# Kernel optimization log

Measured on AMD Instinct MI355X. Metric: run time of the kernel, lower is better.

## Reference

```python
import jax, jax.numpy as jnp
import numpy as np

N_NODES = 50000


def _gcn_norm(edge_index, num_nodes):
    # PyG gcn_norm with add_self_loops=True, edge_weight=1
    loops = jnp.arange(num_nodes, dtype=edge_index.dtype)
    src = jnp.concatenate([edge_index[0], loops])
    dst = jnp.concatenate([edge_index[1], loops])
    deg = jax.ops.segment_sum(jnp.ones_like(dst, dtype=jnp.float32), dst,
                              num_segments=num_nodes)
    deg_inv_sqrt = jnp.where(deg > 0, jax.lax.rsqrt(jnp.maximum(deg, 1.0)), 0.0)
    norm = deg_inv_sqrt[src] * deg_inv_sqrt[dst]  # [E + N]
    return src, dst, norm


def _gcn_conv(x, src, dst, norm, W, b, num_nodes):
    h = x @ W                                 # [N, out] dense transform first
    msg = h[src] * norm[:, None]              # gather + scale, [E+N, out]
    out = jax.ops.segment_sum(msg, dst, num_segments=num_nodes)  # scatter-add
    return out + b


def setup_inputs() -> dict:
    key = jax.random.key(0)
    k1, k2, k3, k4, k5 = jax.random.split(key, 5)
    in_ch, out_ch = 128, 64
    hid = 2 * out_ch
    x = jax.random.normal(k1, (N_NODES, in_ch), dtype=jnp.float32)
    edge_index = jax.random.randint(k2, (2, 800000), 0, N_NODES, dtype=jnp.int64)
    # Glorot init like PyG GCNConv
    W1 = jax.random.normal(k3, (in_ch, hid), dtype=jnp.float32) * (1.0 / np.sqrt(in_ch))
    b1 = jnp.zeros((hid,), dtype=jnp.float32)
    W2 = jax.random.normal(k4, (hid, out_ch), dtype=jnp.float32) * (1.0 / np.sqrt(hid))
    b2 = jnp.zeros((out_ch,), dtype=jnp.float32)
    return {"x": x, "edge_index": edge_index, "W1": W1, "b1": b1,
            "W2": W2, "b2": b2}


def reference(x, edge_index, W1, b1, W2, b2):
    num_nodes = x.shape[0]
    src, dst, norm = _gcn_norm(edge_index, num_nodes)
    h = _gcn_conv(x, src, dst, norm, W1, b1, num_nodes)
    h = jax.nn.relu(h)
    return _gcn_conv(h, src, dst, norm, W2, b2, num_nodes)
```

## Files before the change

### kernel.cpp

```cpp
#include <hip/hip_runtime.h>

#define N_NODES 50000
#define N_EDGES 800000
#define IN_CH   128
#define HID     128
#define OUT_CH  64

#define NBUCK 196
#define BCAP  5120
#define XPAD  136

#define G1_BLOCKS ((N_NODES + 63) / 64)
#define GSPLIT 391

typedef __attribute__((ext_vector_type(8))) short bf16x8;
typedef __attribute__((ext_vector_type(4))) float f32x4;
typedef unsigned short ushort_t;

__device__ __forceinline__ unsigned short f2bf(float f) {
    unsigned u = __float_as_uint(f);
    u += 0x7fffu + ((u >> 16) & 1u);
    return (unsigned short)(u >> 16);
}
__device__ __forceinline__ unsigned pack2(float a, float b) {
    return (unsigned)f2bf(a) | ((unsigned)f2bf(b) << 16);
}
__device__ __forceinline__ float bf_lo(unsigned u) { return __uint_as_float(u << 16); }
__device__ __forceinline__ float bf_hi(unsigned u) { return __uint_as_float(u & 0xffff0000u); }


__global__ __launch_bounds__(256) void k_prep(const float* __restrict__ W1,
                                              const float* __restrict__ W2,
                                              ushort_t* __restrict__ W1t,
                                              ushort_t* __restrict__ W2t,
                                              int* __restrict__ bcur) {
    if (blockIdx.x == 0 && threadIdx.x < NBUCK) bcur[threadIdx.x] = 0;
    int i = blockIdx.x * 256 + threadIdx.x;
    if (i < 128 * 128) {
        int k = i >> 7, c = i & 127;
        W1t[c * 128 + k] = f2bf(W1[k * 128 + c]);
    } else {
        int j = i - 128 * 128;
        if (j < 128 * 64) {
            int k = j >> 6, c = j & 63;
            W2t[c * 128 + k] = f2bf(W2[k * 64 + c]);
        }
    }
}


__global__ __launch_bounds__(256) void k_stage(const int phase, const int tile0,
                                               const int* __restrict__ src,
                                               const int* __restrict__ dst,
                                               int* __restrict__ bcur,
                                               unsigned* __restrict__ rec,
                                               const float* __restrict__ x,
                                               const ushort_t* __restrict__ W1t,
                                               ushort_t* __restrict__ g,
                                               int* __restrict__ row_beg,
                                               int* __restrict__ row_end,
                                               float* __restrict__ dis,
                                               int* __restrict__ col) {
    __shared__ char smem[52224];
    const int tid = threadIdx.x;

    if (blockIdx.x < NBUCK) {
        if (phase == 0) {
            int* lh    = (int*)smem;
            int* gbase = (int*)(smem + 1024);
            for (int i = tid; i < NBUCK; i += 256) lh[i] = 0;
            __syncthreads();
            int base = blockIdx.x * 4096;
#pragma unroll 4
            for (int k = 0; k < 16; ++k) {
                int e = base + k * 256 + tid;
                if (e < N_EDGES) atomicAdd(&lh[dst[e] >> 8], 1);
            }
            __syncthreads();
            for (int i = tid; i < NBUCK; i += 256) {
                int c = lh[i];
                gbase[i] = c ? (i * BCAP + atomicAdd(&bcur[i], c)) : 0;
            }
            __syncthreads();
            for (int i = tid; i < NBUCK; i += 256) lh[i] = 0;
            __syncthreads();
#pragma unroll 4
            for (int k = 0; k < 16; ++k) {
                int e = base + k * 256 + tid;
                if (e < N_EDGES) {
                    int d = dst[e], b = d >> 8;
                    int rk = atomicAdd(&lh[b], 1);
                    int pos = gbase[b] + rk;
                    if (pos < (b + 1) * BCAP)
                        rec[pos] = (unsigned)src[e] | ((unsigned)(d & 255) << 16);
                }
            }
        } else {
            int* lh  = (int*)smem;
            int* cur = lh + 256;
            int* s   = cur + 256;
            const int b = blockIdx.x, t = tid;
            const int lo = b * BCAP;
            const int cnt = min(bcur[b], BCAP);
            const int hi = lo + cnt;

            lh[t] = 0;
            __syncthreads();
            for (int j = lo + t; j < hi; j += 256)
                atomicAdd(&lh[rec[j] >> 16], 1);
            __syncthreads();
            int deg = lh[t];
            s[t] = deg;
            __syncthreads();
            for (int off = 1; off < 256; off <<= 1) {
                int u = (t >= off) ? s[t - off] : 0;
                __syncthreads();
                s[t] += u;
                __syncthreads();
            }
            int gp = lo + s[t] - deg;
            int node = (b << 8) + t;
            if (node < N_NODES) {
                row_beg[node] = gp;
                row_end[node] = gp + deg;
                dis[node] = rsqrtf((float)deg + 1.0f);
            }
            cur[t] = gp;
            __syncthreads();
            for (int j = lo + t; j < hi; j += 256) {
                unsigned r = rec[j];
                int pos = atomicAdd(&cur[r >> 16], 1);
                col[pos] = (int)(r & 0xffffu);
            }
        }
    } else {
        ushort_t* xs = (ushort_t*)smem;
        ushort_t* ws = (ushort_t*)(smem + 17408);
        const int bid = tile0 + (blockIdx.x - NBUCK);
        const int row0 = bid * 64;

        for (int i = tid; i < 64 * 32; i += 256) {
            int r = i >> 5, k4 = (i & 31) << 2;
            int gr = row0 + r;
            float4 v = make_float4(0.f, 0.f, 0.f, 0.f);
            if (gr < N_NODES) v = *(const float4*)&x[(long)gr * IN_CH + k4];
            ushort4 u;
            u.x = f2bf(v.x); u.y = f2bf(v.y); u.z = f2bf(v.z); u.w = f2bf(v.w);
            *(ushort4*)&xs[r * XPAD + k4] = u;
        }
        for (int i = tid; i < 128 * 16; i += 256) {
            int c = i >> 4, seg = i & 15;
            *(uint4*)&ws[c * XPAD + seg * 8] = *(const uint4*)&W1t[c * 128 + seg * 8];
        }
        __syncthreads();

        const int w = tid >> 6, lane = tid & 63;
        const int m = lane & 15, q = lane >> 4;
        const ushort_t* arow = &xs[(w * 16 + m) * XPAD + q * 8];
        const ushort_t* brow = &ws[m * XPAD + q * 8];

        f32x4 acc[8] = {};
#pragma unroll
        for (int k0 = 0; k0 < 128; k0 += 32) {
            bf16x8 a = *(const bf16x8*)(arow + k0);
#pragma unroll
            for (int nt = 0; nt < 8; ++nt) {
                bf16x8 b = *(const bf16x8*)(brow + nt * 16 * XPAD + k0);
                acc[nt] = __builtin_amdgcn_mfma_f32_16x16x32_bf16(a, b, acc[nt], 0, 0, 0);
            }
        }

#pragma unroll
        for (int reg = 0; reg < 4; ++reg) {
            int gr = row0 + w * 16 + q * 4 + reg;
            if (gr < N_NODES) {
#pragma unroll
                for (int nt = 0; nt < 8; ++nt)
                    g[(long)gr * HID + nt * 16 + m] = f2bf(acc[nt][reg]);
            }
        }
    }
}


__global__ __launch_bounds__(256) void k_agg1(const int* __restrict__ row_beg,
                                              const int* __restrict__ row_end,
                                              const int* __restrict__ col,
                                              const float* __restrict__ dis,
                                              const ushort_t* __restrict__ g1,
                                              const float* __restrict__ b1,
                                              ushort_t* __restrict__ a1) {
    int r = blockIdx.x * 4 + (threadIdx.x >> 6);
    if (r >= N_NODES) return;
    const int lane = threadIdx.x & 63;
    const int q = lane >> 4;
    const int seg = lane & 15;
    const int cl = seg << 3;
    const uint4* G = (const uint4*)g1;
    const int beg = row_beg[r], end = row_end[r];

    float acc[8] = {};
    int e = beg + q;
    for (; e + 4 < end; e += 8) {
        int s0 = col[e], s1 = col[e + 4];
        float d0 = dis[s0], d1 = dis[s1];
        uint4 u0 = G[(long)s0 * 16 + seg];
        uint4 u1 = G[(long)s1 * 16 + seg];
        acc[0] += bf_lo(u0.x) * d0; acc[1] += bf_hi(u0.x) * d0;
        acc[2] += bf_lo(u0.y) * d0; acc[3] += bf_hi(u0.y) * d0;
        acc[4] += bf_lo(u0.z) * d0; acc[5] += bf_hi(u0.z) * d0;
        acc[6] += bf_lo(u0.w) * d0; acc[7] += bf_hi(u0.w) * d0;
        acc[0] += bf_lo(u1.x) * d1; acc[1] += bf_hi(u1.x) * d1;
        acc[2] += bf_lo(u1.y) * d1; acc[3] += bf_hi(u1.y) * d1;
        acc[4] += bf_lo(u1.z) * d1; acc[5] += bf_hi(u1.z) * d1;
        acc[6] += bf_lo(u1.w) * d1; acc[7] += bf_hi(u1.w) * d1;
    }
    if (e < end) {
        int s0 = col[e];
        float d0 = dis[s0];
        uint4 u = G[(long)s0 * 16 + seg];
        acc[0] += bf_lo(u.x) * d0; acc[1] += bf_hi(u.x) * d0;
        acc[2] += bf_lo(u.y) * d0; acc[3] += bf_hi(u.y) * d0;
        acc[4] += bf_lo(u.z) * d0; acc[5] += bf_hi(u.z) * d0;
        acc[6] += bf_lo(u.w) * d0; acc[7] += bf_hi(u.w) * d0;
    }
#pragma unroll
    for (int off = 16; off < 64; off <<= 1)
#pragma unroll
        for (int j = 0; j < 8; ++j) acc[j] += __shfl_xor(acc[j], off);

    if (q == 0) {
        const float d = dis[r];
        uint4 u = G[(long)r * 16 + seg];
        acc[0] += bf_lo(u.x) * d; acc[1] += bf_hi(u.x) * d;
        acc[2] += bf_lo(u.y) * d; acc[3] += bf_hi(u.y) * d;
        acc[4] += bf_lo(u.z) * d; acc[5] += bf_hi(u.z) * d;
        acc[6] += bf_lo(u.w) * d; acc[7] += bf_hi(u.w) * d;
        float o[8];
#pragma unroll
        for (int j = 0; j < 8; ++j) o[j] = fmaxf(acc[j] * d + b1[cl + j], 0.f);
        uint4 pw;
        pw.x = pack2(o[0], o[1]); pw.y = pack2(o[2], o[3]);
        pw.z = pack2(o[4], o[5]); pw.w = pack2(o[6], o[7]);
        *(uint4*)&a1[(long)r * HID + cl] = pw;
    }
}


__global__ __launch_bounds__(256) void k_gemm2(const ushort_t* __restrict__ a1,
                                               const ushort_t* __restrict__ W2t,
                                               const float* __restrict__ dis,
                                               ushort_t* __restrict__ g) {
    __shared__ ushort_t xs[64 * XPAD];
    __shared__ ushort_t ws[64 * XPAD];
    const int tid = threadIdx.x;
    const int row0 = blockIdx.x * 64;

    for (int i = tid; i < 64 * 16; i += 256) {
        int r = i >> 4, seg = i & 15;
        int gr = row0 + r;
        uint4 v = make_uint4(0u, 0u, 0u, 0u);
        if (gr < N_NODES) v = *(const uint4*)&a1[(long)gr * HID + seg * 8];
        *(uint4*)&xs[r * XPAD + seg * 8] = v;
    }
    for (int i = tid; i < 64 * 16; i += 256) {
        int c = i >> 4, seg = i & 15;
        *(uint4*)&ws[c * XPAD + seg * 8] = *(const uint4*)&W2t[c * 128 + seg * 8];
    }
    __syncthreads();

    const int w = tid >> 6, lane = tid & 63;
    const int m = lane & 15, q = lane >> 4;
    const ushort_t* arow = &xs[(w * 16 + m) * XPAD + q * 8];
    const ushort_t* brow = &ws[m * XPAD + q * 8];

    f32x4 acc[4] = {};
#pragma unroll
    for (int k0 = 0; k0 < 128; k0 += 32) {
        bf16x8 a = *(const bf16x8*)(arow + k0);
#pragma unroll
        for (int nt = 0; nt < 4; ++nt) {
            bf16x8 b = *(const bf16x8*)(brow + nt * 16 * XPAD + k0);
            acc[nt] = __builtin_amdgcn_mfma_f32_16x16x32_bf16(a, b, acc[nt], 0, 0, 0);
        }
    }

#pragma unroll
    for (int reg = 0; reg < 4; ++reg) {
        int gr = row0 + w * 16 + q * 4 + reg;
        if (gr < N_NODES) {
            float d = dis[gr];
#pragma unroll
            for (int nt = 0; nt < 4; ++nt)
                g[(long)gr * OUT_CH + nt * 16 + m] = f2bf(acc[nt][reg] * d);
        }
    }
}


__global__ __launch_bounds__(256) void k_agg2(const int* __restrict__ row_beg,
                                              const int* __restrict__ row_end,
                                              const int* __restrict__ col,
                                              const float* __restrict__ dis,
                                              const ushort_t* __restrict__ g3,
                                              const float* __restrict__ b2,
                                              float* __restrict__ out) {
    int r = blockIdx.x * 4 + (threadIdx.x >> 6);
    if (r >= N_NODES) return;
    const int lane = threadIdx.x & 63;
    const int q = lane >> 3;
    const int seg = lane & 7;
    const int cl = seg << 3;
    const uint4* G = (const uint4*)g3;
    const int beg = row_beg[r], end = row_end[r];

    float acc[8] = {};
    int e = beg + q;
    for (; e + 8 < end; e += 16) {
        int s0 = col[e], s1 = col[e + 8];
        uint4 u0 = G[(long)s0 * 8 + seg];
        uint4 u1 = G[(long)s1 * 8 + seg];
        acc[0] += bf_lo(u0.x); acc[1] += bf_hi(u0.x);
        acc[2] += bf_lo(u0.y); acc[3] += bf_hi(u0.y);
        acc[4] += bf_lo(u0.z); acc[5] += bf_hi(u0.z);
        acc[6] += bf_lo(u0.w); acc[7] += bf_hi(u0.w);
        acc[0] += bf_lo(u1.x); acc[1] += bf_hi(u1.x);
        acc[2] += bf_lo(u1.y); acc[3] += bf_hi(u1.y);
        acc[4] += bf_lo(u1.z); acc[5] += bf_hi(u1.z);
        acc[6] += bf_lo(u1.w); acc[7] += bf_hi(u1.w);
    }
    if (e < end) {
        int s = col[e];
        uint4 u = G[(long)s * 8 + seg];
        acc[0] += bf_lo(u.x); acc[1] += bf_hi(u.x);
        acc[2] += bf_lo(u.y); acc[3] += bf_hi(u.y);
        acc[4] += bf_lo(u.z); acc[5] += bf_hi(u.z);
        acc[6] += bf_lo(u.w); acc[7] += bf_hi(u.w);
    }
#pragma unroll
    for (int off = 8; off < 64; off <<= 1)
#pragma unroll
        for (int j = 0; j < 8; ++j) acc[j] += __shfl_xor(acc[j], off);

    if (q == 0) {
        uint4 u = G[(long)r * 8 + seg];
        acc[0] += bf_lo(u.x); acc[1] += bf_hi(u.x);
        acc[2] += bf_lo(u.y); acc[3] += bf_hi(u.y);
        acc[4] += bf_lo(u.z); acc[5] += bf_hi(u.z);
        acc[6] += bf_lo(u.w); acc[7] += bf_hi(u.w);
        const float d = dis[r];
        float4 o0, o1;
        o0.x = acc[0] * d + b2[cl + 0];
        o0.y = acc[1] * d + b2[cl + 1];
        o0.z = acc[2] * d + b2[cl + 2];
        o0.w = acc[3] * d + b2[cl + 3];
        o1.x = acc[4] * d + b2[cl + 4];
        o1.y = acc[5] * d + b2[cl + 5];
        o1.z = acc[6] * d + b2[cl + 6];
        o1.w = acc[7] * d + b2[cl + 7];
        *(float4*)&out[(long)r * OUT_CH + cl] = o0;
        *(float4*)&out[(long)r * OUT_CH + cl + 4] = o1;
    }
}


extern "C" void kernel_launch(void* const* d_in, const int* in_sizes, int n_in,
                              void* d_out, int out_size, void* d_ws, size_t ws_size,
                              hipStream_t stream) {
    const float* x   = (const float*)d_in[0];
    const int*   ei  = (const int*)d_in[1];
    const float* W1  = (const float*)d_in[2];
    const float* b1  = (const float*)d_in[3];
    const float* W2  = (const float*)d_in[4];
    const float* b2  = (const float*)d_in[5];
    float* out = (float*)d_out;

    const int* src = ei;
    const int* dst = ei + N_EDGES;

    char* p = (char*)d_ws;
    unsigned* rec = (unsigned*)p;         p += (long)NBUCK * BCAP * 4;
    int* col     = (int*)p;               p += (long)NBUCK * BCAP * 4;
    int* row_beg = (int*)p;               p += 50048 * 4;
    int* row_end = (int*)p;               p += 50048 * 4;
    int* bcur    = (int*)p;               p += 256 * 4;
    float* dis   = (float*)p;             p += 50048 * 4;
    ushort_t* W1t = (ushort_t*)p;         p += 128 * 128 * 2;
    ushort_t* W2t = (ushort_t*)p;         p += 128 * 64 * 2;
    ushort_t* g1  = (ushort_t*)p;         p += (long)N_NODES * HID * 2;
    ushort_t* a1  = (ushort_t*)p;         p += (long)N_NODES * HID * 2;
    ushort_t* g3  = (ushort_t*)p;

    const int B = 256;

    k_prep<<<96, B, 0, stream>>>(W1, W2, W1t, W2t, bcur);
    k_stage<<<NBUCK + GSPLIT, B, 0, stream>>>(0, 0, src, dst, bcur, rec,
                                              x, W1t, g1, row_beg, row_end, dis, col);
    k_stage<<<NBUCK + (G1_BLOCKS - GSPLIT), B, 0, stream>>>(1, GSPLIT, src, dst, bcur, rec,
                                              x, W1t, g1, row_beg, row_end, dis, col);
    k_agg1<<<(N_NODES + 3) / 4, B, 0, stream>>>(row_beg, row_end, col, dis, g1, b1, a1);
    k_gemm2<<<(N_NODES + 63) / 64, B, 0, stream>>>(a1, W2t, dis, g3);
    k_agg2<<<(N_NODES + 3) / 4, B, 0, stream>>>(row_beg, row_end, col, dis, g3, b2, out);
}
```

Baseline: 177.3 us.

## Fuse layer-1 aggregation with layer-2 GEMM via shared-memory tile

Merges the first aggregation kernel and the second dense transform into one kernel. Each block aggregates 16 rows (4 per wave), writes the ReLU'd bf16 rows into a shared tile, then runs MFMA against W2 read directly from global memory to produce g3. This removes the a1 round trip through global memory and one kernel launch. In exchange, each wave handles 4 rows serially, which may reduce latency hiding in the gather. W2t is also re-read from global/L2 by every block instead of being staged in LDS.

```diff
diff --git a/kernel.cpp b/kernel.cpp
--- a/kernel.cpp
+++ b/kernel.cpp
@@ -183,117 +183,92 @@
 }
 
 
-__global__ __launch_bounds__(256) void k_agg1(const int* __restrict__ row_beg,
-                                              const int* __restrict__ row_end,
-                                              const int* __restrict__ col,
-                                              const float* __restrict__ dis,
-                                              const ushort_t* __restrict__ g1,
-                                              const float* __restrict__ b1,
-                                              ushort_t* __restrict__ a1) {
-    int r = blockIdx.x * 4 + (threadIdx.x >> 6);
-    if (r >= N_NODES) return;
-    const int lane = threadIdx.x & 63;
+__global__ __launch_bounds__(256) void k_agg1g2(const int* __restrict__ row_beg,
+                                                const int* __restrict__ row_end,
+                                                const int* __restrict__ col,
+                                                const float* __restrict__ dis,
+                                                const ushort_t* __restrict__ g1,
+                                                const float* __restrict__ b1,
+                                                const ushort_t* __restrict__ W2t,
+                                                ushort_t* __restrict__ g3) {
+    __shared__ ushort_t hs[16 * XPAD];
+    const int tid = threadIdx.x;
+    const int w = tid >> 6, lane = tid & 63;
     const int q = lane >> 4;
     const int seg = lane & 15;
     const int cl = seg << 3;
     const uint4* G = (const uint4*)g1;
-    const int beg = row_beg[r], end = row_end[r];
-
-    float acc[8] = {};
-    int e = beg + q;
-    for (; e + 4 < end; e += 8) {
-        int s0 = col[e], s1 = col[e + 4];
-        float d0 = dis[s0], d1 = dis[s1];
-        uint4 u0 = G[(long)s0 * 16 + seg];
-        uint4 u1 = G[(long)s1 * 16 + seg];
-        acc[0] += bf_lo(u0.x) * d0; acc[1] += bf_hi(u0.x) * d0;
-        acc[2] += bf_lo(u0.y) * d0; acc[3] += bf_hi(u0.y) * d0;
-        acc[4] += bf_lo(u0.z) * d0; acc[5] += bf_hi(u0.z) * d0;
-        acc[6] += bf_lo(u0.w) * d0; acc[7] += bf_hi(u0.w) * d0;
-        acc[0] += bf_lo(u1.x) * d1; acc[1] += bf_hi(u1.x) * d1;
-        acc[2] += bf_lo(u1.y) * d1; acc[3] += bf_hi(u1.y) * d1;
-        acc[4] += bf_lo(u1.z) * d1; acc[5] += bf_hi(u1.z) * d1;
-        acc[6] += bf_lo(u1.w) * d1; acc[7] += bf_hi(u1.w) * d1;
-    }
-    if (e < end) {
-        int s0 = col[e];
-        float d0 = dis[s0];
-        uint4 u = G[(long)s0 * 16 + seg];
-        acc[0] += bf_lo(u.x) * d0; acc[1] += bf_hi(u.x) * d0;
-        acc[2] += bf_lo(u.y) * d0; acc[3] += bf_hi(u.y) * d0;
-        acc[4] += bf_lo(u.z) * d0; acc[5] += bf_hi(u.z) * d0;
-        acc[6] += bf_lo(u.w) * d0; acc[7] += bf_hi(u.w) * d0;
-    }
-#pragma unroll
-    for (int off = 16; off < 64; off <<= 1)
-#pragma unroll
-        for (int j = 0; j < 8; ++j) acc[j] += __shfl_xor(acc[j], off);
-
-    if (q == 0) {
-        const float d = dis[r];
-        uint4 u = G[(long)r * 16 + seg];
-        acc[0] += bf_lo(u.x) * d; acc[1] += bf_hi(u.x) * d;
-        acc[2] += bf_lo(u.y) * d; acc[3] += bf_hi(u.y) * d;
-        acc[4] += bf_lo(u.z) * d; acc[5] += bf_hi(u.z) * d;
-        acc[6] += bf_lo(u.w) * d; acc[7] += bf_hi(u.w) * d;
-        float o[8];
-#pragma unroll
-        for (int j = 0; j < 8; ++j) o[j] = fmaxf(acc[j] * d + b1[cl + j], 0.f);
-        uint4 pw;
-        pw.x = pack2(o[0], o[1]); pw.y = pack2(o[2], o[3]);
-        pw.z = pack2(o[4], o[5]); pw.w = pack2(o[6], o[7]);
-        *(uint4*)&a1[(long)r * HID + cl] = pw;
-    }
-}
-
-
-__global__ __launch_bounds__(256) void k_gemm2(const ushort_t* __restrict__ a1,
-                                               const ushort_t* __restrict__ W2t,
-                                               const float* __restrict__ dis,
-                                               ushort_t* __restrict__ g) {
-    __shared__ ushort_t xs[64 * XPAD];
-    __shared__ ushort_t ws[64 * XPAD];
-    const int tid = threadIdx.x;
-    const int row0 = blockIdx.x * 64;
-
-    for (int i = tid; i < 64 * 16; i += 256) {
-        int r = i >> 4, seg = i & 15;
-        int gr = row0 + r;
-        uint4 v = make_uint4(0u, 0u, 0u, 0u);
-        if (gr < N_NODES) v = *(const uint4*)&a1[(long)gr * HID + seg * 8];
-        *(uint4*)&xs[r * XPAD + seg * 8] = v;
-    }
-    for (int i = tid; i < 64 * 16; i += 256) {
-        int c = i >> 4, seg = i & 15;
-        *(uint4*)&ws[c * XPAD + seg * 8] = *(const uint4*)&W2t[c * 128 + seg * 8];
+    const int r0 = blockIdx.x * 16;
+
+    for (int rr = 0; rr < 4; ++rr) {
+        const int r = r0 + w * 4 + rr;
+        const int beg = row_beg[r], end = row_end[r];
+
+        float acc[8] = {};
+        int e = beg + q;
+        for (; e + 4 < end; e += 8) {
+            int s0 = col[e], s1 = col[e + 4];
+            float d0 = dis[s0], d1 = dis[s1];
+            uint4 u0 = G[(long)s0 * 16 + seg];
+            uint4 u1 = G[(long)s1 * 16 + seg];
+            acc[0] += bf_lo(u0.x) * d0; acc[1] += bf_hi(u0.x) * d0;
+            acc[2] += bf_lo(u0.y) * d0; acc[3] += bf_hi(u0.y) * d0;
+            acc[4] += bf_lo(u0.z) * d0; acc[5] += bf_hi(u0.z) * d0;
+            acc[6] += bf_lo(u0.w) * d0; acc[7] += bf_hi(u0.w) * d0;
+            acc[0] += bf_lo(u1.x) * d1; acc[1] += bf_hi(u1.x) * d1;
+            acc[2] += bf_lo(u1.y) * d1; acc[3] += bf_hi(u1.y) * d1;
+            acc[4] += bf_lo(u1.z) * d1; acc[5] += bf_hi(u1.z) * d1;
+            acc[6] += bf_lo(u1.w) * d1; acc[7] += bf_hi(u1.w) * d1;
+        }
+        if (e < end) {
+            int s0 = col[e];
+            float d0 = dis[s0];
+            uint4 u = G[(long)s0 * 16 + seg];
+            acc[0] += bf_lo(u.x) * d0; acc[1] += bf_hi(u.x) * d0;
+            acc[2] += bf_lo(u.y) * d0; acc[3] += bf_hi(u.y) * d0;
+            acc[4] += bf_lo(u.z) * d0; acc[5] += bf_hi(u.z) * d0;
+            acc[6] += bf_lo(u.w) * d0; acc[7] += bf_hi(u.w) * d0;
+        }
+#pragma unroll
+        for (int off = 16; off < 64; off <<= 1)
+#pragma unroll
+            for (int j = 0; j < 8; ++j) acc[j] += __shfl_xor(acc[j], off);
+
+        if (q == 0) {
+            const float d = dis[r];
+            uint4 u = G[(long)r * 16 + seg];
+            acc[0] += bf_lo(u.x) * d; acc[1] += bf_hi(u.x) * d;
+            acc[2] += bf_lo(u.y) * d; acc[3] += bf_hi(u.y) * d;
+            acc[4] += bf_lo(u.z) * d; acc[5] += bf_hi(u.z) * d;
+            acc[6] += bf_lo(u.w) * d; acc[7] += bf_hi(u.w) * d;
+            float o[8];
+#pragma unroll
+            for (int j = 0; j < 8; ++j) o[j] = fmaxf(acc[j] * d + b1[cl + j], 0.f);
+            uint4 pw;
+            pw.x = pack2(o[0], o[1]); pw.y = pack2(o[2], o[3]);
+            pw.z = pack2(o[4], o[5]); pw.w = pack2(o[6], o[7]);
+            *(uint4*)&hs[(w * 4 + rr) * XPAD + cl] = pw;
+        }
     }
     __syncthreads();
 
-    const int w = tid >> 6, lane = tid & 63;
-    const int m = lane & 15, q = lane >> 4;
-    const ushort_t* arow = &xs[(w * 16 + m) * XPAD + q * 8];
-    const ushort_t* brow = &ws[m * XPAD + q * 8];
-
-    f32x4 acc[4] = {};
+    const int m = lane & 15;
+    const ushort_t* arow = &hs[m * XPAD + q * 8];
+    const ushort_t* brow = &W2t[(w * 16 + m) * 128 + q * 8];
+
+    f32x4 acc2 = {};
 #pragma unroll
     for (int k0 = 0; k0 < 128; k0 += 32) {
         bf16x8 a = *(const bf16x8*)(arow + k0);
-#pragma unroll
-        for (int nt = 0; nt < 4; ++nt) {
-            bf16x8 b = *(const bf16x8*)(brow + nt * 16 * XPAD + k0);
-            acc[nt] = __builtin_amdgcn_mfma_f32_16x16x32_bf16(a, b, acc[nt], 0, 0, 0);
-        }
+        bf16x8 b = *(const bf16x8*)(brow + k0);
+        acc2 = __builtin_amdgcn_mfma_f32_16x16x32_bf16(a, b, acc2, 0, 0, 0);
     }
 
 #pragma unroll
     for (int reg = 0; reg < 4; ++reg) {
-        int gr = row0 + w * 16 + q * 4 + reg;
-        if (gr < N_NODES) {
-            float d = dis[gr];
-#pragma unroll
-            for (int nt = 0; nt < 4; ++nt)
-                g[(long)gr * OUT_CH + nt * 16 + m] = f2bf(acc[nt][reg] * d);
-        }
+        int gr = r0 + q * 4 + reg;
+        float d = dis[gr];
+        g3[(long)gr * OUT_CH + w * 16 + m] = f2bf(acc2[reg] * d);
     }
 }
 
@@ -390,6 +365,7 @@
     ushort_t* g1  = (ushort_t*)p;         p += (long)N_NODES * HID * 2;
     ushort_t* a1  = (ushort_t*)p;         p += (long)N_NODES * HID * 2;
     ushort_t* g3  = (ushort_t*)p;
+    (void)a1;
 
     const int B = 256;
 
@@ -398,7 +374,6 @@
                                               x, W1t, g1, row_beg, row_end, dis, col);
     k_stage<<<NBUCK + (G1_BLOCKS - GSPLIT), B, 0, stream>>>(1, GSPLIT, src, dst, bcur, rec,
                                               x, W1t, g1, row_beg, row_end, dis, col);
-    k_agg1<<<(N_NODES + 3) / 4, B, 0, stream>>>(row_beg, row_end, col, dis, g1, b1, a1);
-    k_gemm2<<<(N_NODES + 63) / 64, B, 0, stream>>>(a1, W2t, dis, g3);
+    k_agg1g2<<<3125, B, 0, stream>>>(row_beg, row_end, col, dis, g1, b1, W2t, g3);
     k_agg2<<<(N_NODES + 3) / 4, B, 0, stream>>>(row_beg, row_end, col, dis, g3, b2, out);
 }
```

Result: no change. 176.6 us (-0.4%).
